# Kernel tuning notes

Hardware: AMD Instinct MI355X
Metric: run time of the kernel (lower is better)

## Reference

```python
import jax, jax.numpy as jnp
import numpy as np

BSZ, SEQ, EMBED, HEADS = 2, 2048, 1024, 16
HEAD_DIM = EMBED // HEADS


def setup_inputs() -> dict:
    key = jax.random.key(0)
    ks = jax.random.split(key, 12)
    s = 0.02
    inp = {
        'query': jax.random.normal(ks[0], (BSZ, SEQ, EMBED), jnp.float32),
        'key':   jax.random.normal(ks[1], (BSZ, SEQ, EMBED), jnp.float32),
        'value': jax.random.normal(ks[2], (BSZ, SEQ, EMBED), jnp.float32),
        # causal mask, broadcast over batch: positions with 0 are masked to -inf
        'mask': jnp.broadcast_to(jnp.tril(jnp.ones((SEQ, SEQ), jnp.int32)), (BSZ, SEQ, SEQ)),
        'Wq': jax.random.normal(ks[3], (EMBED, EMBED), jnp.float32) * s,
        'bq': jnp.zeros((EMBED,), jnp.float32),
        'Wk': jax.random.normal(ks[4], (EMBED, EMBED), jnp.float32) * s,
        'bk': jnp.zeros((EMBED,), jnp.float32),
        'Wv': jax.random.normal(ks[5], (EMBED, EMBED), jnp.float32) * s,
        'bv': jnp.zeros((EMBED,), jnp.float32),
        'Wo': jax.random.normal(ks[6], (EMBED, EMBED), jnp.float32) * s,
        'bo': jnp.zeros((EMBED,), jnp.float32),
    }
    return inp


def reference(query, key, value, mask, Wq, bq, Wk, bk, Wv, bv, Wo, bo):
    bsz, seq_len, embed_dim = query.shape
    scaling = HEAD_DIM ** -0.5

    def proj(x, W, b):  # torch Linear: x @ W.T + b, then split heads -> [b, h, s, d]
        y = jnp.einsum('bse,fe->bsf', x, W) + b
        return y.reshape(bsz, -1, HEADS, HEAD_DIM).transpose(0, 2, 1, 3)

    q = proj(query, Wq, bq)
    k = proj(key, Wk, bk)
    v = proj(value, Wv, bv)

    scores = jnp.einsum('bhqd,bhkd->bhqk', q, k) * scaling  # [b, h, s, s]
    scores = jnp.where(mask[:, None, :, :] == 0, -jnp.inf, scores)
    attn = jax.nn.softmax(scores, axis=-1)  # dropout p=0.0 -> identity
    vals = jnp.einsum('bhqk,bhkd->bhqd', attn, v)
    vals = vals.transpose(0, 2, 1, 3).reshape(bsz, seq_len, embed_dim)
    out = jnp.einsum('bse,fe->bsf', vals, Wo) + bo
    return out
```

## Files before the change

### kernel.cpp

```cpp
#include <hip/hip_runtime.h>
#include <hip/hip_bf16.h>


typedef __bf16 bf16;
typedef bf16 bf16x4 __attribute__((ext_vector_type(4)));
typedef bf16 bf16x8 __attribute__((ext_vector_type(8)));
typedef float f32x4 __attribute__((ext_vector_type(4)));

constexpr int BSZ = 2, SEQ = 2048, EMBED = 1024, HEADS = 16, HDIM = 64;
constexpr int MTOT = BSZ * SEQ;
constexpr int KDIM = EMBED;
constexpr float QSCALE = 0.125f * 1.4426950408889634f;

constexpr size_t XSZ = (size_t)MTOT * EMBED;
constexpr size_t WSZ = (size_t)EMBED * EMBED;

__device__ inline void load_lds16(const bf16* g, bf16* l) {
    __builtin_amdgcn_global_load_lds(
        (const __attribute__((address_space(1))) unsigned int*)g,
        (__attribute__((address_space(3))) unsigned int*)l, 16, 0, 0);
}

__global__ __launch_bounds__(256) void cvt_bf16(
    const float* __restrict__ x0, const float* __restrict__ x1, const float* __restrict__ x2,
    const float* __restrict__ w0, const float* __restrict__ w1,
    const float* __restrict__ w2, const float* __restrict__ w3,
    bf16* __restrict__ dst) {
    const size_t i = ((size_t)blockIdx.x * blockDim.x + threadIdx.x) * 8;
    const float* src;
    size_t off;
    if (i < 3 * XSZ) {
        const int s = (int)(i >> 22);
        src = s == 0 ? x0 : (s == 1 ? x1 : x2);
        off = i & (XSZ - 1);
    } else {
        const size_t j = i - 3 * XSZ;
        const int s = (int)(j >> 20);
        src = s == 0 ? w0 : (s == 1 ? w1 : (s == 2 ? w2 : w3));
        off = j & (WSZ - 1);
    }
    float4 a = *(const float4*)(src + off);
    float4 b = *(const float4*)(src + off + 4);
    bf16x8 v = {(bf16)a.x, (bf16)a.y, (bf16)a.z, (bf16)a.w,
                (bf16)b.x, (bf16)b.y, (bf16)b.z, (bf16)b.w};
    *(bf16x8*)(dst + i) = v;
}

struct MMCtx {
    int wave, lane, quad, l16, wm, wn, lrow, lcol;
};
__device__ inline MMCtx mm_ctx() {
    MMCtx c;
    const int tid = threadIdx.x;
    c.wave = tid >> 6; c.lane = tid & 63;
    c.quad = c.lane >> 4; c.l16 = c.lane & 15;
    c.wm = (c.wave & 1) * 64; c.wn = (c.wave >> 1) * 64;
    c.lrow = c.lane >> 3; c.lcol = (c.lane & 7) * 8;
    return c;
}

template <bool SWAP>
__device__ inline void mm_loop(const bf16* __restrict__ A, const bf16* __restrict__ W,
                               int rowA0, int rowB0, const MMCtx& c,
                               bf16 (*As)[64], bf16 (*Bs)[64], f32x4 acc[4][4]) {
    for (int k0 = 0; k0 < KDIM; k0 += 64) {
        for (int i = 0; i < 4; ++i) {
            const int r0 = (c.wave * 4 + i) * 8;
            const int row = r0 + c.lrow;
            const int gcol = (c.lcol - 8 * row) & 63;
            load_lds16(&A[(size_t)(rowA0 + row) * KDIM + k0 + gcol], &As[r0][0]);
            load_lds16(&W[(size_t)(rowB0 + row) * KDIM + k0 + gcol], &Bs[r0][0]);
        }
        __syncthreads();
        for (int ks = 0; ks < 64; ks += 32) {
            bf16x8 af[4], bfr[4];
            for (int mt = 0; mt < 4; ++mt) {
                const int row = c.wm + mt * 16 + c.l16;
                af[mt] = *(const bf16x8*)&As[row][(ks + c.quad * 8 + 8 * row) & 63];
            }
            for (int nt = 0; nt < 4; ++nt) {
                const int row = c.wn + nt * 16 + c.l16;
                bfr[nt] = *(const bf16x8*)&Bs[row][(ks + c.quad * 8 + 8 * row) & 63];
            }
            for (int mt = 0; mt < 4; ++mt)
                for (int nt = 0; nt < 4; ++nt)
                    acc[mt][nt] = SWAP
                        ? __builtin_amdgcn_mfma_f32_16x16x32_bf16(bfr[nt], af[mt], acc[mt][nt], 0, 0, 0)
                        : __builtin_amdgcn_mfma_f32_16x16x32_bf16(af[mt], bfr[nt], acc[mt][nt], 0, 0, 0);
        }
        __syncthreads();
    }
}

__global__ __launch_bounds__(256) void gemm_qkv(
    const bf16* __restrict__ Xq, const bf16* __restrict__ Xk, const bf16* __restrict__ Xv,
    const bf16* __restrict__ Wq, const bf16* __restrict__ Wk, const bf16* __restrict__ Wv,
    const float* __restrict__ bq, const float* __restrict__ bk, const float* __restrict__ bv,
    bf16* __restrict__ Qp, bf16* __restrict__ Kp, bf16* __restrict__ Vtp) {
    __shared__ bf16 As[128][64];
    __shared__ bf16 Bs[128][64];

    const int z = blockIdx.z;
    const bf16* A     = z == 0 ? Xq : (z == 1 ? Xk : Xv);
    const bf16* W     = z == 0 ? Wq : (z == 1 ? Wk : Wv);
    const float* bias = z == 0 ? bq : (z == 1 ? bk : bv);
    const float scale = z == 0 ? QSCALE : 1.0f;

    const MMCtx c = mm_ctx();
    const int rowA0 = blockIdx.x * 128;
    const int rowB0 = blockIdx.y * 128;
    f32x4 acc[4][4] = {};

    if (z < 2) {
        mm_loop<true>(A, W, rowA0, rowB0, c, As, Bs, acc);
        bf16* dst = z == 0 ? Qp : Kp;
        for (int mt = 0; mt < 4; ++mt) {
            const int xrow = rowA0 + c.wm + mt * 16 + c.l16;
            const int b = xrow >> 11, s = xrow & (SEQ - 1);
            for (int nt = 0; nt < 4; ++nt) {
                const int f0 = rowB0 + c.wn + nt * 16 + c.quad * 4;
                const float4 bb = *(const float4*)&bias[f0];
                const int h = f0 >> 6, d0 = f0 & (HDIM - 1);
                f32x4 a = acc[mt][nt];
                bf16x4 pk = {(bf16)((a[0] + bb.x) * scale), (bf16)((a[1] + bb.y) * scale),
                             (bf16)((a[2] + bb.z) * scale), (bf16)((a[3] + bb.w) * scale)};
                *(bf16x4*)&dst[(((size_t)(b * HEADS + h)) * SEQ + s) * HDIM + d0] = pk;
            }
        }
    } else {
        mm_loop<false>(A, W, rowA0, rowB0, c, As, Bs, acc);
        for (int nt = 0; nt < 4; ++nt) {
            const int f = rowB0 + c.wn + nt * 16 + c.l16;
            const float bb = bias[f];
            const int h = f >> 6, d = f & (HDIM - 1);
            for (int mt = 0; mt < 4; ++mt) {
                const int xrow0 = rowA0 + c.wm + mt * 16 + c.quad * 4;
                const int b = xrow0 >> 11, s0 = xrow0 & (SEQ - 1);
                f32x4 a = acc[mt][nt];
                bf16x4 pk = {(bf16)(a[0] + bb), (bf16)(a[1] + bb),
                             (bf16)(a[2] + bb), (bf16)(a[3] + bb)};
                *(bf16x4*)&Vtp[(((size_t)(b * HEADS + h)) * HDIM + d) * SEQ + s0] = pk;
            }
        }
    }
}

__global__ __launch_bounds__(256) void gemm_out(const bf16* __restrict__ A,
                                                const bf16* __restrict__ W,
                                                const float* __restrict__ bias,
                                                float* __restrict__ C) {
    __shared__ bf16 As[128][64];
    __shared__ bf16 Bs[64][64];

    const int tid = threadIdx.x;
    const int wave = tid >> 6, lane = tid & 63;
    const int quad = lane >> 4, l16 = lane & 15;
    const int wm = (wave & 1) * 64, wn = (wave >> 1) * 32;
    const int lrow = lane >> 3, lcol = (lane & 7) * 8;
    const int rowA0 = blockIdx.x * 128;
    const int rowB0 = blockIdx.y * 64;

    f32x4 acc[4][2] = {};
    for (int k0 = 0; k0 < KDIM; k0 += 64) {
        for (int i = 0; i < 4; ++i) {
            const int r0 = (wave * 4 + i) * 8;
            const int row = r0 + lrow;
            const int gcol = (lcol - 8 * row) & 63;
            load_lds16(&A[(size_t)(rowA0 + row) * KDIM + k0 + gcol], &As[r0][0]);
        }
        for (int i = 0; i < 2; ++i) {
            const int r0 = (wave * 2 + i) * 8;
            const int row = r0 + lrow;
            const int gcol = (lcol - 8 * row) & 63;
            load_lds16(&W[(size_t)(rowB0 + row) * KDIM + k0 + gcol], &Bs[r0][0]);
        }
        __syncthreads();
        for (int ks = 0; ks < 64; ks += 32) {
            bf16x8 af[4], bfr[2];
            for (int mt = 0; mt < 4; ++mt) {
                const int row = wm + mt * 16 + l16;
                af[mt] = *(const bf16x8*)&As[row][(ks + quad * 8 + 8 * row) & 63];
            }
            for (int nt = 0; nt < 2; ++nt) {
                const int row = wn + nt * 16 + l16;
                bfr[nt] = *(const bf16x8*)&Bs[row][(ks + quad * 8 + 8 * row) & 63];
            }
            for (int mt = 0; mt < 4; ++mt)
                for (int nt = 0; nt < 2; ++nt)
                    acc[mt][nt] = __builtin_amdgcn_mfma_f32_16x16x32_bf16(
                        bfr[nt], af[mt], acc[mt][nt], 0, 0, 0);
        }
        __syncthreads();
    }

    for (int mt = 0; mt < 4; ++mt) {
        const int row = rowA0 + wm + mt * 16 + l16;
        for (int nt = 0; nt < 2; ++nt) {
            const int f0 = rowB0 + wn + nt * 16 + quad * 4;
            const float4 bb = *(const float4*)&bias[f0];
            f32x4 a = acc[mt][nt];
            float4 v = {a[0] + bb.x, a[1] + bb.y, a[2] + bb.z, a[3] + bb.w};
            *(float4*)&C[(size_t)row * EMBED + f0] = v;
        }
    }
}

__global__ __launch_bounds__(128) void attn_flash(const bf16* __restrict__ Q,
                                                  const bf16* __restrict__ K,
                                                  const bf16* __restrict__ Vt,
                                                  bf16* __restrict__ O) {
    const int l = blockIdx.x;
    const int a = l & 7, s = l >> 3;
    const int bh = 4 * a + (s >> 5);
    const int p = s & 31;
    const int wave = threadIdx.x >> 6, lane = threadIdx.x & 63;
    const int quad = lane >> 4, l16 = lane & 15;

    const bf16* Qh = Q + (size_t)bh * SEQ * HDIM;
    const bf16* Kh = K + (size_t)bh * SEQ * HDIM;
    const bf16* Vh = Vt + (size_t)bh * HDIM * SEQ;

    __shared__ bf16 Ks[2][64][64];
    __shared__ bf16 Vs[2][64][64];
    __shared__ bf16 Ps[2][16][64];

    const int b = bh >> 4, h = bh & 15;

    auto stage = [&](int buf, int k0) {
#pragma unroll
        for (int cc = 0; cc < 4; ++cc) {
            const int row = cc * 16 + wave * 8 + (lane >> 3);
            const int g = (((lane & 7) * 8) - 8 * row) & 63;
            load_lds16(&Kh[(size_t)(k0 + row) * HDIM + g], &Ks[buf][cc * 16 + wave * 8][0]);
            load_lds16(&Vh[(size_t)row * SEQ + k0 + g], &Vs[buf][cc * 16 + wave * 8][0]);
        }
    };

    bf16x8 ones;
#pragma unroll
    for (int i = 0; i < 8; ++i) ones[i] = (bf16)1.0f;

#pragma unroll 1
    for (int phase = 0; phase < 2; ++phase) {
        const int qt = phase == 0 ? (63 - p) : p;
        const int qw = qt * 32 + wave * 16;
        const int nk = (qt >> 1) + 1;

        bf16x8 qf[2];
#pragma unroll
        for (int ks = 0; ks < 2; ++ks)
            qf[ks] = *(const bf16x8*)&Qh[(size_t)(qw + l16) * HDIM + ks * 32 + quad * 8];

        f32x4 ot[4] = {};
        f32x4 lacc = {};

        stage(0, 0);
#pragma unroll 1
        for (int it = 0; it < nk; ++it) {
            const int k0 = it * 64;
            const int buf = it & 1;
            __syncthreads();
            if (it + 1 < nk) stage(buf ^ 1, k0 + 64);

            if (k0 < qw + 16) {
                f32x4 st[4] = {};
#pragma unroll
                for (int mt = 0; mt < 4; ++mt) {
                    const int krow = mt * 16 + l16;
#pragma unroll
                    for (int ks = 0; ks < 2; ++ks) {
                        const int colL = (ks * 32 + 8 * (quad + krow)) & 63;
                        bf16x8 kf = *(const bf16x8*)&Ks[buf][krow][colL];
                        st[mt] = __builtin_amdgcn_mfma_f32_16x16x32_bf16(kf, qf[ks], st[mt], 0, 0, 0);
                    }
                }
                if (k0 + 63 >= qw) {
                    const int q = qw + l16;
#pragma unroll
                    for (int mt = 0; mt < 4; ++mt) {
                        const int key = k0 + mt * 16 + quad * 4;
#pragma unroll
                        for (int r = 0; r < 4; ++r)
                            if (key + r > q) st[mt][r] = -__builtin_inff();
                    }
                }
#pragma unroll
                for (int mt = 0; mt < 4; ++mt) {
                    f32x4 pv;
#pragma unroll
                    for (int r = 0; r < 4; ++r) pv[r] = exp2f(st[mt][r]);
                    bf16x4 pk = {(bf16)pv[0], (bf16)pv[1], (bf16)pv[2], (bf16)pv[3]};
                    *(bf16x4*)&Ps[wave][l16][(mt * 16 + quad * 4 + 8 * l16) & 63] = pk;
                }
#pragma unroll
                for (int c = 0; c < 2; ++c) {
                    bf16x8 pf = *(const bf16x8*)&Ps[wave][l16][(c * 32 + quad * 8 + 8 * l16) & 63];
                    lacc = __builtin_amdgcn_mfma_f32_16x16x32_bf16(ones, pf, lacc, 0, 0, 0);
#pragma unroll
                    for (int dt = 0; dt < 4; ++dt) {
                        const int drow = dt * 16 + l16;
                        const int colL = (c * 32 + quad * 8 + 8 * drow) & 63;
                        bf16x8 vf = *(const bf16x8*)&Vs[buf][drow][colL];
                        ot[dt] = __builtin_amdgcn_mfma_f32_16x16x32_bf16(vf, pf, ot[dt], 0, 0, 0);
                    }
                }
            }
        }
        __syncthreads();

        const float inv = 1.f / lacc[0];
        const int sq = qw + l16;
#pragma unroll
        for (int dt = 0; dt < 4; ++dt) {
            bf16x4 pk = {(bf16)(ot[dt][0] * inv), (bf16)(ot[dt][1] * inv),
                         (bf16)(ot[dt][2] * inv), (bf16)(ot[dt][3] * inv)};
            *(bf16x4*)&O[((size_t)(b * SEQ + sq)) * EMBED + h * HDIM + dt * 16 + quad * 4] = pk;
        }
    }
}

extern "C" void kernel_launch(void* const* d_in, const int* in_sizes, int n_in,
                              void* d_out, int out_size, void* d_ws, size_t ws_size,
                              hipStream_t stream) {
    const float* q_in = (const float*)d_in[0];
    const float* k_in = (const float*)d_in[1];
    const float* v_in = (const float*)d_in[2];
    const float* Wq = (const float*)d_in[4];
    const float* bq = (const float*)d_in[5];
    const float* Wk = (const float*)d_in[6];
    const float* bk = (const float*)d_in[7];
    const float* Wv = (const float*)d_in[8];
    const float* bv = (const float*)d_in[9];
    const float* Wo = (const float*)d_in[10];
    const float* bo = (const float*)d_in[11];

    bf16* ws = (bf16*)d_ws;
    bf16* Xb  = ws;
    bf16* Wb  = ws + 3 * XSZ;
    bf16* Qp  = ws + 3 * XSZ + 4 * WSZ;
    bf16* Kp  = Qp + XSZ;
    bf16* Vtp = Kp + XSZ;
    bf16* AO  = ws;

    const size_t total = 3 * XSZ + 4 * WSZ;
    dim3 bb(256);
    cvt_bf16<<<dim3((unsigned)(total / 8 / 256)), bb, 0, stream>>>(
        q_in, k_in, v_in, Wq, Wk, Wv, Wo, ws);
    gemm_qkv<<<dim3(MTOT / 128, EMBED / 128, 3), bb, 0, stream>>>(
        Xb, Xb + XSZ, Xb + 2 * XSZ, Wb, Wb + WSZ, Wb + 2 * WSZ,
        bq, bk, bv, Qp, Kp, Vtp);
    attn_flash<<<dim3(1024), dim3(128), 0, stream>>>(Qp, Kp, Vtp, AO);
    gemm_out<<<dim3(MTOT / 128, EMBED / 64), bb, 0, stream>>>(
        AO, Wb + 3 * WSZ, bo, (float*)d_out);
}
```

Measured before the change: 246.0 us.

## Drop LDS staging in attention; per-wave causal-balanced query tiles with direct global loads

```diff
diff --git a/kernel.cpp b/kernel.cpp
--- a/kernel.cpp
+++ b/kernel.cpp
@@ -205,14 +205,14 @@
     }
 }
 
-__global__ __launch_bounds__(128) void attn_flash(const bf16* __restrict__ Q,
+__global__ __launch_bounds__(256) void attn_flash(const bf16* __restrict__ Q,
                                                   const bf16* __restrict__ K,
                                                   const bf16* __restrict__ Vt,
                                                   bf16* __restrict__ O) {
     const int l = blockIdx.x;
     const int a = l & 7, s = l >> 3;
     const int bh = 4 * a + (s >> 5);
-    const int p = s & 31;
+    const int m = s & 31;
     const int wave = threadIdx.x >> 6, lane = threadIdx.x & 63;
     const int quad = lane >> 4, l16 = lane & 15;
 
@@ -220,102 +220,78 @@
     const bf16* Kh = K + (size_t)bh * SEQ * HDIM;
     const bf16* Vh = Vt + (size_t)bh * HDIM * SEQ;
 
-    __shared__ bf16 Ks[2][64][64];
-    __shared__ bf16 Vs[2][64][64];
-    __shared__ bf16 Ps[2][16][64];
+    __shared__ bf16 Ps[4][16][64];
 
     const int b = bh >> 4, h = bh & 15;
 
-    auto stage = [&](int buf, int k0) {
-#pragma unroll
-        for (int cc = 0; cc < 4; ++cc) {
-            const int row = cc * 16 + wave * 8 + (lane >> 3);
-            const int g = (((lane & 7) * 8) - 8 * row) & 63;
-            load_lds16(&Kh[(size_t)(k0 + row) * HDIM + g], &Ks[buf][cc * 16 + wave * 8][0]);
-            load_lds16(&Vh[(size_t)row * SEQ + k0 + g], &Vs[buf][cc * 16 + wave * 8][0]);
-        }
-    };
+    const int qt = (wave == 0) ? m : (wave == 1) ? (63 - m)
+                 : (wave == 2) ? (64 + m) : (127 - m);
+    const int qw = qt * 16;
+    const int nk = (qt >> 2) + 1;
+
+    bf16x8 qf[2];
+#pragma unroll
+    for (int ks = 0; ks < 2; ++ks)
+        qf[ks] = *(const bf16x8*)&Qh[(size_t)(qw + l16) * HDIM + ks * 32 + quad * 8];
+
+    f32x4 ot[4] = {};
+    f32x4 lacc = {};
 
     bf16x8 ones;
 #pragma unroll
     for (int i = 0; i < 8; ++i) ones[i] = (bf16)1.0f;
 
 #pragma unroll 1
-    for (int phase = 0; phase < 2; ++phase) {
-        const int qt = phase == 0 ? (63 - p) : p;
-        const int qw = qt * 32 + wave * 16;
-        const int nk = (qt >> 1) + 1;
-
-        bf16x8 qf[2];
-#pragma unroll
-        for (int ks = 0; ks < 2; ++ks)
-            qf[ks] = *(const bf16x8*)&Qh[(size_t)(qw + l16) * HDIM + ks * 32 + quad * 8];
-
-        f32x4 ot[4] = {};
-        f32x4 lacc = {};
-
-        stage(0, 0);
-#pragma unroll 1
-        for (int it = 0; it < nk; ++it) {
-            const int k0 = it * 64;
-            const int buf = it & 1;
-            __syncthreads();
-            if (it + 1 < nk) stage(buf ^ 1, k0 + 64);
-
-            if (k0 < qw + 16) {
-                f32x4 st[4] = {};
-#pragma unroll
-                for (int mt = 0; mt < 4; ++mt) {
-                    const int krow = mt * 16 + l16;
-#pragma unroll
-                    for (int ks = 0; ks < 2; ++ks) {
-                        const int colL = (ks * 32 + 8 * (quad + krow)) & 63;
-                        bf16x8 kf = *(const bf16x8*)&Ks[buf][krow][colL];
-                        st[mt] = __builtin_amdgcn_mfma_f32_16x16x32_bf16(kf, qf[ks], st[mt], 0, 0, 0);
-                    }
-                }
-                if (k0 + 63 >= qw) {
-                    const int q = qw + l16;
-#pragma unroll
-                    for (int mt = 0; mt < 4; ++mt) {
-                        const int key = k0 + mt * 16 + quad * 4;
-#pragma unroll
-                        for (int r = 0; r < 4; ++r)
-                            if (key + r > q) st[mt][r] = -__builtin_inff();
-                    }
-                }
-#pragma unroll
-                for (int mt = 0; mt < 4; ++mt) {
-                    f32x4 pv;
-#pragma unroll
-                    for (int r = 0; r < 4; ++r) pv[r] = exp2f(st[mt][r]);
-                    bf16x4 pk = {(bf16)pv[0], (bf16)pv[1], (bf16)pv[2], (bf16)pv[3]};
-                    *(bf16x4*)&Ps[wave][l16][(mt * 16 + quad * 4 + 8 * l16) & 63] = pk;
-                }
-#pragma unroll
-                for (int c = 0; c < 2; ++c) {
-                    bf16x8 pf = *(const bf16x8*)&Ps[wave][l16][(c * 32 + quad * 8 + 8 * l16) & 63];
-                    lacc = __builtin_amdgcn_mfma_f32_16x16x32_bf16(ones, pf, lacc, 0, 0, 0);
-#pragma unroll
-                    for (int dt = 0; dt < 4; ++dt) {
-                        const int drow = dt * 16 + l16;
-                        const int colL = (c * 32 + quad * 8 + 8 * drow) & 63;
-                        bf16x8 vf = *(const bf16x8*)&Vs[buf][drow][colL];
-                        ot[dt] = __builtin_amdgcn_mfma_f32_16x16x32_bf16(vf, pf, ot[dt], 0, 0, 0);
-                    }
-                }
-            }
-        }
-        __syncthreads();
-
-        const float inv = 1.f / lacc[0];
-        const int sq = qw + l16;
-#pragma unroll
-        for (int dt = 0; dt < 4; ++dt) {
-            bf16x4 pk = {(bf16)(ot[dt][0] * inv), (bf16)(ot[dt][1] * inv),
-                         (bf16)(ot[dt][2] * inv), (bf16)(ot[dt][3] * inv)};
-            *(bf16x4*)&O[((size_t)(b * SEQ + sq)) * EMBED + h * HDIM + dt * 16 + quad * 4] = pk;
-        }
+    for (int it = 0; it < nk; ++it) {
+        const int k0 = it * 64;
+
+        f32x4 st[4] = {};
+#pragma unroll
+        for (int mt = 0; mt < 4; ++mt) {
+            const int krow = k0 + mt * 16 + l16;
+#pragma unroll
+            for (int ks = 0; ks < 2; ++ks) {
+                bf16x8 kf = *(const bf16x8*)&Kh[(size_t)krow * HDIM + ks * 32 + quad * 8];
+                st[mt] = __builtin_amdgcn_mfma_f32_16x16x32_bf16(kf, qf[ks], st[mt], 0, 0, 0);
+            }
+        }
+        if (it == nk - 1) {
+            const int q = qw + l16;
+#pragma unroll
+            for (int mt = 0; mt < 4; ++mt) {
+                const int key = k0 + mt * 16 + quad * 4;
+#pragma unroll
+                for (int r = 0; r < 4; ++r)
+                    if (key + r > q) st[mt][r] = -__builtin_inff();
+            }
+        }
+#pragma unroll
+        for (int mt = 0; mt < 4; ++mt) {
+            f32x4 pv;
+#pragma unroll
+            for (int r = 0; r < 4; ++r) pv[r] = exp2f(st[mt][r]);
+            bf16x4 pk = {(bf16)pv[0], (bf16)pv[1], (bf16)pv[2], (bf16)pv[3]};
+            *(bf16x4*)&Ps[wave][l16][(mt * 16 + quad * 4 + 8 * l16) & 63] = pk;
+        }
+#pragma unroll
+        for (int c = 0; c < 2; ++c) {
+            bf16x8 pf = *(const bf16x8*)&Ps[wave][l16][(c * 32 + quad * 8 + 8 * l16) & 63];
+            lacc = __builtin_amdgcn_mfma_f32_16x16x32_bf16(ones, pf, lacc, 0, 0, 0);
+#pragma unroll
+            for (int dt = 0; dt < 4; ++dt) {
+                bf16x8 vf = *(const bf16x8*)&Vh[(size_t)(dt * 16 + l16) * SEQ + k0 + c * 32 + quad * 8];
+                ot[dt] = __builtin_amdgcn_mfma_f32_16x16x32_bf16(vf, pf, ot[dt], 0, 0, 0);
+            }
+        }
+    }
+
+    const float inv = 1.f / lacc[0];
+    const int sq = qw + l16;
+#pragma unroll
+    for (int dt = 0; dt < 4; ++dt) {
+        bf16x4 pk = {(bf16)(ot[dt][0] * inv), (bf16)(ot[dt][1] * inv),
+                     (bf16)(ot[dt][2] * inv), (bf16)(ot[dt][3] * inv)};
+        *(bf16x4*)&O[((size_t)(b * SEQ + sq)) * EMBED + h * HDIM + dt * 16 + quad * 4] = pk;
     }
 }
 
@@ -349,7 +325,7 @@
     gemm_qkv<<<dim3(MTOT / 128, EMBED / 128, 3), bb, 0, stream>>>(
         Xb, Xb + XSZ, Xb + 2 * XSZ, Wb, Wb + WSZ, Wb + 2 * WSZ,
         bq, bk, bv, Qp, Kp, Vtp);
-    attn_flash<<<dim3(1024), dim3(128), 0, stream>>>(Qp, Kp, Vtp, AO);
+    attn_flash<<<dim3(1024), bb, 0, stream>>>(Qp, Kp, Vtp, AO);
     gemm_out<<<dim3(MTOT / 128, EMBED / 64), bb, 0, stream>>>(
         AO, Wb + 3 * WSZ, bo, (float*)d_out);
 }
```

Result: slower. 329.2 us (+33.8%).
